# Kernel tuning notes

Hardware: AMD Instinct MI355X
Metric: run time of the kernel (lower is better)

## Reference

```python
import jax, jax.numpy as jnp
import numpy as np

SHARPNESS = 1000.0   # sigmoid temperature from source: *1000.0
BIAS = 0.008         # shadow acne bias from source: -0.008
FILTER_SIZE = 1      # 3x3 PCF
SHADOW_STEP = 1


def setup_inputs() -> dict:
    key = jax.random.key(0)
    k1, k2, k3 = jax.random.split(key, 3)
    N, H, W, K, S = 8, 1024, 1024, 1, 2048
    # light-view depth buffer (fragments_from_light.zbuf), K=1 squeezed
    light_zbuf = jax.random.uniform(k1, (N, S, S), dtype=jnp.float32)
    depth_z = jax.random.uniform(k2, (N, H, W, K), dtype=jnp.float32)
    # rounded integer light-screen coords per camera pixel: [..., 0]=x, [..., 1]=y
    xy = jax.random.randint(k3, (N, H, W, K, 2), 0, S, dtype=jnp.int32)
    return {"light_zbuf": light_zbuf, "depth_z": depth_z, "xy": xy, "image_size": S}


def reference(light_zbuf, depth_z, xy, image_size):
    N, H, W, K = depth_z.shape
    b = jnp.arange(N, dtype=jnp.int32)[:, None, None, None]  # broadcast batch index
    x = xy[..., 0]  # [N,H,W,K]
    y = xy[..., 1]
    aa = depth_z - BIAS
    vis = jnp.zeros_like(depth_z)
    # 3x3 PCF: gather clamped neighbors in the light zbuf, soft depth test, accumulate
    for ii in range(-FILTER_SIZE, FILTER_SIZE + 1):
        for jj in range(-FILTER_SIZE, FILTER_SIZE + 1):
            yi = jnp.clip(y + ii * SHADOW_STEP, 0, image_size - 1)
            xi = jnp.clip(x + jj * SHADOW_STEP, 0, image_size - 1)
            bb = light_zbuf[b, yi, xi]  # [N,H,W,K] gather
            vis = vis + jax.nn.sigmoid((bb - aa) * SHARPNESS)
    return vis / float((1 + 2 * FILTER_SIZE) ** 2)
```

## Files before the change

### kernel.cpp

```cpp
#include <hip/hip_runtime.h>


#define SHARPNESS 1000.0f
#define BIAS 0.008f
#define S2LOG2E 1442.6950408889634f

#define S_IMG   2048
#define NBATCH  8
#define HWK     (1 << 20)
#define TSH     6
#define TPS     32
#define BPB     (TPS * TPS)
#define CAP     1792
#define RPT     7
#define STW     66
#define PXB     8192
#define P1T     1024
#define PPT     (PXB / P1T)
#define SENT    0xFFFFFFFFu

typedef int      i4v __attribute__((ext_vector_type(4)));
typedef float    f2v __attribute__((ext_vector_type(2)));
typedef float    f4v __attribute__((ext_vector_type(4)));
typedef unsigned u2v __attribute__((ext_vector_type(2)));
typedef unsigned u4v __attribute__((ext_vector_type(4)));

__device__ __forceinline__ float sigf(float bb, float a) {
    const float t = (a - bb) * S2LOG2E;
    return __builtin_amdgcn_rcpf(1.0f + exp2f(t));
}

__global__ __launch_bounds__(P1T, 2) void p1_bin(
    const int* __restrict__ xy_raw, const float* __restrict__ depth,
    u2v* __restrict__ slab, float* __restrict__ out ,
    unsigned* __restrict__ gcur, int b0)
{
    __shared__ u2v      srec[PXB];
    __shared__ unsigned scn[BPB];
    __shared__ unsigned lbase[BPB];
    __shared__ unsigned gbse[BPB];

    const int blk = blockIdx.x;
    const int bl  = blk >> 7;
    const int sub = blk & 127;
    const int tid = threadIdx.x;
    scn[tid] = 0;
    __syncthreads();

    const size_t pb_g = (size_t)(b0 + bl) * HWK + (size_t)sub * PXB;
    const i4v* xq = (const i4v*)xy_raw + pb_g / 2;
    const f2v* dq = (const f2v*)depth  + pb_g / 2;

    unsigned pk[PPT]; float dd[PPT];
#pragma unroll
    for (int j = 0; j < PPT / 2; ++j) {
        const i4v q = __builtin_nontemporal_load(&xq[j * P1T + tid]);
        const f2v d = __builtin_nontemporal_load(&dq[j * P1T + tid]);
        pk[2 * j]     = (unsigned)q.x | ((unsigned)q.y << 11);
        pk[2 * j + 1] = (unsigned)q.z | ((unsigned)q.w << 11);
        dd[2 * j] = d.x; dd[2 * j + 1] = d.y;
        atomicAdd(&scn[((q.y >> TSH) << 5) | (q.x >> TSH)], 1u);
        atomicAdd(&scn[((q.w >> TSH) << 5) | (q.z >> TSH)], 1u);
    }
    __syncthreads();

    const unsigned creg = scn[tid];
    for (int ofs = 1; ofs < BPB; ofs <<= 1) {
        const unsigned u = (tid >= ofs) ? scn[tid - ofs] : 0u;
        __syncthreads();
        scn[tid] += u;
        __syncthreads();
    }
    const unsigned lb = scn[tid] - creg;
    lbase[tid] = lb;
    gbse[tid]  = atomicAdd(&gcur[bl * BPB + tid], (creg + 7u) & ~7u);
    scn[tid]   = lb;
    __syncthreads();

    u2v* px2 = (u2v*)(out + pb_g);
#pragma unroll
    for (int j = 0; j < PPT / 2; ++j) {
        u2v pi;
#pragma unroll
        for (int e = 0; e < 2; ++e) {
            const unsigned w = pk[2 * j + e];
            const int x = (int)(w & 0x7FFu), y = (int)(w >> 11);
            const int bn = ((y >> TSH) << 5) | (x >> TSH);
            const unsigned r = atomicAdd(&scn[bn], 1u);
            u2v rec;
            rec.x = (unsigned)(x & 63) | ((unsigned)(y & 63) << 6);
            rec.y = __float_as_uint(dd[2 * j + e]);
            srec[r] = rec;
            const unsigned pos = gbse[bn] + (r - lbase[bn]);
            const unsigned slot = (pos < CAP)
                ? (unsigned)(bl * BPB + bn) * CAP + pos : SENT;
            if (e == 0) pi.x = slot; else pi.y = slot;
        }
        px2[j * P1T + tid] = pi;
    }
    __syncthreads();

    const int wid = tid >> 6, lane = tid & 63;
    u2v* slb = slab + (size_t)bl * BPB * CAP;
    for (int bn = wid * 64; bn < wid * 64 + 64; ++bn) {
        const int c   = (int)(scn[bn] - lbase[bn]);
        const int len = (c + 7) & ~7;
        const int src = (int)lbase[bn];
        const int gp  = (int)gbse[bn];
        u2v* dst = slb + (size_t)bn * CAP;
        for (int k = lane; k < len; k += 64) {
            const int pos = gp + k;
            if (pos < CAP) {
                u2v r;
                if (k < c) r = srec[src + k];
                else { r.x = 0u; r.y = 0x7F800000u; }
                dst[pos] = r;
            }
        }
    }
}

__global__ __launch_bounds__(256, 8) void p2_tile(
    const float* __restrict__ zbuf, const u2v* __restrict__ slab,
    float* __restrict__ vis, const unsigned* __restrict__ gcur, int b0)
{
    __shared__ float zt[STW * STW];
    const int gb  = blockIdx.x;
    const int tid = threadIdx.x;
    const int bl  = gb >> 10;
    const int t   = gb & (BPB - 1);
    const int tx  = t & 31, ty = t >> 5;
    const float* zb = zbuf + (size_t)(b0 + bl) * ((size_t)S_IMG * S_IMG);
    const int x0 = tx * 64 - 1, y0 = ty * 64 - 1;

    const int n   = min((int)gcur[gb], CAP);
    const int nc  = n - 1;
    const int ncc = max(nc, 0);
    const u2v* sl = slab + (size_t)gb * CAP;

    u2v Rc[RPT];
#pragma unroll
    for (int j = 0; j < RPT; ++j)
        Rc[j] = sl[min(j * 256 + tid, ncc)];

    for (int i = tid; i < STW * STW; i += 256) {
        const int r  = i / STW, c = i - r * STW;
        const int gy = min(max(y0 + r, 0), S_IMG - 1);
        const int gx = min(max(x0 + c, 0), S_IMG - 1);
        zt[i] = zb[(size_t)gy * S_IMG + gx];
    }
    __syncthreads();

    float* vb = vis + (size_t)gb * CAP;
#pragma unroll
    for (int j = 0; j < RPT; ++j) {
        const unsigned w = Rc[j].x;
        const float a  = __uint_as_float(Rc[j].y) - BIAS;
        const float* p = zt + (int)((w >> 6) & 63u) * STW + (int)(w & 63u);
        const float v =
              sigf(p[0],           a) + sigf(p[1],           a) + sigf(p[2],           a)
            + sigf(p[STW],         a) + sigf(p[STW + 1],     a) + sigf(p[STW + 2],     a)
            + sigf(p[2 * STW],     a) + sigf(p[2 * STW + 1], a) + sigf(p[2 * STW + 2], a);
        const int k = j * 256 + tid;
        if (k <= nc) vb[k] = v * (1.0f / 9.0f);
    }
}

__global__ __launch_bounds__(256) void p3_out(
    const float* __restrict__ visf, float* __restrict__ out,
    const float* __restrict__ zbuf, const float* __restrict__ depth,
    const int* __restrict__ xy_raw, int b0)
{
    const int tid = threadIdx.x;
    const size_t pxbase = (size_t)b0 * HWK + (size_t)blockIdx.x * 4096;
    const u4v* px4 = (const u4v*)(out + pxbase);

    u4v P[4];
#pragma unroll
    for (int j = 0; j < 4; ++j)
        P[j] = px4[j * 256 + tid];

    f4v V[4];
#pragma unroll
    for (int j = 0; j < 4; ++j) {
#pragma unroll
        for (int e = 0; e < 4; ++e) {
            const unsigned pi = P[j][e];
            float v;
            if (pi != SENT) {
                v = visf[pi];
            } else {
                const size_t il = pxbase + (size_t)(j * 256 + tid) * 4 + e;
                const int batch = (int)(il >> 20);
                const float a = depth[il] - BIAS;
                const int x = xy_raw[2 * il], y = xy_raw[2 * il + 1];
                const float* zbb = zbuf + (size_t)batch * ((size_t)S_IMG * S_IMG);
                float vv = 0.0f;
                for (int ii = -1; ii <= 1; ++ii) {
                    const int yi = min(max(y + ii, 0), S_IMG - 1);
                    const float* row = zbb + (size_t)yi * S_IMG;
                    for (int jj = -1; jj <= 1; ++jj)
                        vv += sigf(row[min(max(x + jj, 0), S_IMG - 1)], a);
                }
                v = vv * (1.0f / 9.0f);
            }
            V[j][e] = v;
        }
    }

    f4v* o4 = (f4v*)(out + pxbase);
#pragma unroll
    for (int j = 0; j < 4; ++j)
        __builtin_nontemporal_store(V[j], &o4[j * 256 + tid]);
}

__global__ __launch_bounds__(256) void pcf_shadow_generic(
    const float* __restrict__ zbuf, const float* __restrict__ depth_z,
    const int2* __restrict__ xy, const int* __restrict__ image_size_p,
    float* __restrict__ out, int total, int zbuf_elems)
{
    const int i = blockIdx.x * blockDim.x + threadIdx.x;
    if (i >= total) return;
    const int S  = *image_size_p;
    const int SS = S * S;
    const int N  = zbuf_elems / SS;
    const int hwk = total / N;
    const int b   = i / hwk;
    const float a = depth_z[i] - BIAS;
    const int2 p  = xy[i];
    const float* base = zbuf + (size_t)b * (size_t)SS;
    float vis = 0.0f;
#pragma unroll
    for (int ii = -1; ii <= 1; ++ii) {
        const int yi = min(max(p.y + ii, 0), S - 1);
        const float* row = base + (size_t)yi * (size_t)S;
#pragma unroll
        for (int jj = -1; jj <= 1; ++jj) {
            const int xi = min(max(p.x + jj, 0), S - 1);
            vis += 1.0f / (1.0f + __expf((a - row[xi]) * SHARPNESS));
        }
    }
    out[i] = vis * (1.0f / 9.0f);
}

extern "C" void kernel_launch(void* const* d_in, const int* in_sizes, int n_in,
                              void* d_out, int out_size, void* d_ws, size_t ws_size,
                              hipStream_t stream) {
    const float* zbuf     = (const float*)d_in[0];
    const float* depth_z  = (const float*)d_in[1];
    const int*   xy_raw   = (const int*)d_in[2];
    const int*   img_size = (const int*)d_in[3];
    float*       out      = (float*)d_out;

    const int zbuf_elems = in_sizes[0];
    const int total      = in_sizes[1];

    if (zbuf_elems == NBATCH * S_IMG * S_IMG && total == NBATCH * HWK) {
        const size_t slab_pb = (size_t)BPB * CAP * 8ull;
        const size_t vis_pb  = (size_t)BPB * CAP * 4ull;
        const size_t per_b   = slab_pb + vis_pb + (size_t)BPB * 4ull;
        int nb = 0;
        if      (ws_size >= 8 * per_b) nb = 8;
        else if (ws_size >= 4 * per_b) nb = 4;
        else if (ws_size >= 2 * per_b) nb = 2;
        else if (ws_size >= 1 * per_b) nb = 1;

        if (nb) {
            u2v*      slab = (u2v*)d_ws;
            float*    vis  = (float*)((char*)d_ws + (size_t)nb * slab_pb);
            unsigned* gcur = (unsigned*)((char*)d_ws + (size_t)nb * (slab_pb + vis_pb));
            for (int b0 = 0; b0 < NBATCH; b0 += nb) {
                hipMemsetAsync(gcur, 0, (size_t)nb * BPB * 4ull, stream);
                p1_bin <<<nb * 128, P1T, 0, stream>>>(xy_raw, depth_z, slab, out, gcur, b0);
                p2_tile<<<nb * BPB, 256, 0, stream>>>(zbuf, slab, vis, gcur, b0);
                p3_out <<<nb * 256, 256, 0, stream>>>(vis, out, zbuf, depth_z, xy_raw, b0);
            }
            return;
        }
    }
    const int block = 256;
    const int grid  = (total + block - 1) / block;
    pcf_shadow_generic<<<grid, block, 0, stream>>>(zbuf, depth_z, (const int2*)xy_raw,
                                                   img_size, out, total, zbuf_elems);
}
```

Baseline: 394.4 us.

## Store tile visibility in place in the slab, shrink bin capacity, and double the bin chunk

p2_tile now writes each record's visibility into the depth slot of its slab record instead of a separate vis buffer, and p3_out reads it back from there. This removes one workspace array. Bin capacity CAP drops from 1792 to 1408 (RPT from 7 to 6), which shrinks the slab and p2's register footprint. Binning now handles 16384 pixels per block with occupancy 1, using about 140 KB of LDS, and gcur is indexed per global batch and zeroed with a single memset instead of one per batch group. The trade-offs are more overflow pixels sent to the slow sentinel path in p3 if a tile exceeds the smaller capacity, lower p1 occupancy, and 8-byte-strided visibility gathers in p3.

```diff
diff --git a/kernel.cpp b/kernel.cpp
--- a/kernel.cpp
+++ b/kernel.cpp
@@ -11,12 +11,13 @@
 #define TSH     6
 #define TPS     32
 #define BPB     (TPS * TPS)
-#define CAP     1792
-#define RPT     7
+#define CAP     1408
+#define RPT     6
 #define STW     66
-#define PXB     8192
+#define PXB     16384
 #define P1T     1024
 #define PPT     (PXB / P1T)
+#define BLKB    (HWK / PXB)
 #define SENT    0xFFFFFFFFu
 
 typedef int      i4v __attribute__((ext_vector_type(4)));
@@ -30,7 +31,7 @@
     return __builtin_amdgcn_rcpf(1.0f + exp2f(t));
 }
 
-__global__ __launch_bounds__(P1T, 2) void p1_bin(
+__global__ __launch_bounds__(P1T, 1) void p1_bin(
     const int* __restrict__ xy_raw, const float* __restrict__ depth,
     u2v* __restrict__ slab, float* __restrict__ out ,
     unsigned* __restrict__ gcur, int b0)
@@ -41,8 +42,8 @@
     __shared__ unsigned gbse[BPB];
 
     const int blk = blockIdx.x;
-    const int bl  = blk >> 7;
-    const int sub = blk & 127;
+    const int bl  = blk >> 6;
+    const int sub = blk & (BLKB - 1);
     const int tid = threadIdx.x;
     scn[tid] = 0;
     __syncthreads();
@@ -73,7 +74,7 @@
     }
     const unsigned lb = scn[tid] - creg;
     lbase[tid] = lb;
-    gbse[tid]  = atomicAdd(&gcur[bl * BPB + tid], (creg + 7u) & ~7u);
+    gbse[tid]  = atomicAdd(&gcur[(b0 + bl) * BPB + tid], (creg + 7u) & ~7u);
     scn[tid]   = lb;
     __syncthreads();
 
@@ -121,8 +122,8 @@
 }
 
 __global__ __launch_bounds__(256, 8) void p2_tile(
-    const float* __restrict__ zbuf, const u2v* __restrict__ slab,
-    float* __restrict__ vis, const unsigned* __restrict__ gcur, int b0)
+    const float* __restrict__ zbuf, u2v* __restrict__ slab,
+    const unsigned* __restrict__ gcur, int b0)
 {
     __shared__ float zt[STW * STW];
     const int gb  = blockIdx.x;
@@ -133,10 +134,10 @@
     const float* zb = zbuf + (size_t)(b0 + bl) * ((size_t)S_IMG * S_IMG);
     const int x0 = tx * 64 - 1, y0 = ty * 64 - 1;
 
-    const int n   = min((int)gcur[gb], CAP);
+    const int n   = min((int)gcur[(b0 + bl) * BPB + t], CAP);
     const int nc  = n - 1;
     const int ncc = max(nc, 0);
-    const u2v* sl = slab + (size_t)gb * CAP;
+    u2v* sl = slab + (size_t)gb * CAP;
 
     u2v Rc[RPT];
 #pragma unroll
@@ -151,7 +152,7 @@
     }
     __syncthreads();
 
-    float* vb = vis + (size_t)gb * CAP;
+    float* slf = (float*)sl;
 #pragma unroll
     for (int j = 0; j < RPT; ++j) {
         const unsigned w = Rc[j].x;
@@ -162,12 +163,12 @@
             + sigf(p[STW],         a) + sigf(p[STW + 1],     a) + sigf(p[STW + 2],     a)
             + sigf(p[2 * STW],     a) + sigf(p[2 * STW + 1], a) + sigf(p[2 * STW + 2], a);
         const int k = j * 256 + tid;
-        if (k <= nc) vb[k] = v * (1.0f / 9.0f);
+        if (k <= nc) slf[2 * k + 1] = v * (1.0f / 9.0f);
     }
 }
 
 __global__ __launch_bounds__(256) void p3_out(
-    const float* __restrict__ visf, float* __restrict__ out,
+    const float* __restrict__ slabf, float* __restrict__ out,
     const float* __restrict__ zbuf, const float* __restrict__ depth,
     const int* __restrict__ xy_raw, int b0)
 {
@@ -188,7 +189,7 @@
             const unsigned pi = P[j][e];
             float v;
             if (pi != SENT) {
-                v = visf[pi];
+                v = slabf[2 * (size_t)pi + 1];
             } else {
                 const size_t il = pxbase + (size_t)(j * 256 + tid) * 4 + e;
                 const int batch = (int)(il >> 20);
@@ -257,23 +258,22 @@
 
     if (zbuf_elems == NBATCH * S_IMG * S_IMG && total == NBATCH * HWK) {
         const size_t slab_pb = (size_t)BPB * CAP * 8ull;
-        const size_t vis_pb  = (size_t)BPB * CAP * 4ull;
-        const size_t per_b   = slab_pb + vis_pb + (size_t)BPB * 4ull;
+        const size_t gcur_b  = (size_t)NBATCH * BPB * 4ull;
         int nb = 0;
-        if      (ws_size >= 8 * per_b) nb = 8;
-        else if (ws_size >= 4 * per_b) nb = 4;
-        else if (ws_size >= 2 * per_b) nb = 2;
-        else if (ws_size >= 1 * per_b) nb = 1;
+        if      (ws_size >= 8 * slab_pb + gcur_b) nb = 8;
+        else if (ws_size >= 4 * slab_pb + gcur_b) nb = 4;
+        else if (ws_size >= 2 * slab_pb + gcur_b) nb = 2;
+        else if (ws_size >= 1 * slab_pb + gcur_b) nb = 1;
 
         if (nb) {
             u2v*      slab = (u2v*)d_ws;
-            float*    vis  = (float*)((char*)d_ws + (size_t)nb * slab_pb);
-            unsigned* gcur = (unsigned*)((char*)d_ws + (size_t)nb * (slab_pb + vis_pb));
+            unsigned* gcur = (unsigned*)((char*)d_ws + (size_t)nb * slab_pb);
+            hipMemsetAsync(gcur, 0, gcur_b, stream);
             for (int b0 = 0; b0 < NBATCH; b0 += nb) {
-                hipMemsetAsync(gcur, 0, (size_t)nb * BPB * 4ull, stream);
-                p1_bin <<<nb * 128, P1T, 0, stream>>>(xy_raw, depth_z, slab, out, gcur, b0);
-                p2_tile<<<nb * BPB, 256, 0, stream>>>(zbuf, slab, vis, gcur, b0);
-                p3_out <<<nb * 256, 256, 0, stream>>>(vis, out, zbuf, depth_z, xy_raw, b0);
+                p1_bin <<<nb * BLKB, P1T, 0, stream>>>(xy_raw, depth_z, slab, out, gcur, b0);
+                p2_tile<<<nb * BPB,  256, 0, stream>>>(zbuf, slab, gcur, b0);
+                p3_out <<<nb * 256,  256, 0, stream>>>((const float*)slab, out,
+                                                       zbuf, depth_z, xy_raw, b0);
             }
             return;
         }
```

Measured after the change: 407.0 us. 1.03x slower.
